# Kernel optimization log

Measured on AMD Instinct MI355X. Metric: run time of the kernel, lower is better.

The kernel has to match this reference:

```python
import jax, jax.numpy as jnp
import numpy as np

LN_EPS = 1e-5
BN_EPS = 1e-5
ATTN_EPS = 1e-6

def _ln(x, g, b):
    m = x.mean(-1, keepdims=True)
    v = x.var(-1, keepdims=True)
    return (x - m) / jnp.sqrt(v + LN_EPS) * g + b

def setup_inputs() -> dict:
    key = jax.random.key(0)
    ks = jax.random.split(key, 16)
    B, C, N = 4, 256, 8192
    s = 0.05
    def rn(k, shape, scale=1.0):
        return jax.random.normal(k, shape, jnp.float32) * scale
    return {
        "x1": rn(ks[0], (B, C, N)),
        "x2": rn(ks[1], (B, C, N)),
        "Wq": rn(ks[2], (C, C), s), "bq": rn(ks[3], (C,), s),
        "Wk": rn(ks[4], (C, C), s), "bk": rn(ks[5], (C,), s),
        "Wv": rn(ks[6], (C, C), s), "bv": rn(ks[7], (C,), s),
        "threshold": jnp.array([0.1], jnp.float32),
        "W1": rn(ks[8], (2 * C, 2 * C), s),
        "W2": rn(ks[9], (C, 2 * C), s),
        "g1": jnp.ones((C,), jnp.float32), "b1": jnp.zeros((C,), jnp.float32),
        "g2": jnp.ones((C,), jnp.float32), "b2": jnp.zeros((C,), jnp.float32),
        "Wa": rn(ks[10], (C, C), s), "ba": rn(ks[11], (C,), s),
        "bn_g": jnp.ones((C,), jnp.float32), "bn_b": jnp.zeros((C,), jnp.float32),
        "bn_m": jnp.zeros((C,), jnp.float32), "bn_v": jnp.ones((C,), jnp.float32),
    }

def reference(x1, x2, Wq, bq, Wk, bk, Wv, bv, threshold, W1, W2,
              g1, b1, g2, b2, Wa, ba, bn_g, bn_b, bn_m, bn_v):
    B, C, N = x1.shape
    H = 4
    d = C // H
    def conv1x1(x, W, b):  # nn.Conv1d(C, C, 1): [B,C,N] -> [B,C,N]
        return jnp.einsum('bcn,oc->bon', x, W) + b[:, None]
    # projections -> [B, N, H, d]
    q = conv1x1(x1, Wq, bq).transpose(0, 2, 1).reshape(B, N, H, d)
    k = conv1x1(x2, Wk, bk).transpose(0, 2, 1).reshape(B, N, H, d)
    v = conv1x1(x2, Wv, bv).transpose(0, 2, 1).reshape(B, N, H, d)
    # DynamicSparseLinearAttention
    Q = jax.nn.elu(q) + 1.0
    K = jax.nn.elu(k) + 1.0
    S = v.shape[1]
    vals = v / S
    KV = jnp.einsum('nshd,nshv->nhdv', K, vals)               # [B,H,d,d]
    scores = jnp.einsum('nlhd,nhd->nlh', Q, K.sum(axis=1))    # [B,N,H]
    sparse = jnp.where(scores > threshold[0], scores, 0.0)
    Z = 1.0 / (sparse + ATTN_EPS)
    msg = jnp.einsum('nlhd,nhdv,nlh->nlhv', Q, KV, Z) * S     # [B,N,H,d]
    # view [B,N,C]; the transpose(1,2).transpose(1,2) in torch cancels
    msg = msg.reshape(B, N, H * d)
    msg = _ln(msg, g1, b1)
    msg = jnp.concatenate([x1.transpose(0, 2, 1), msg], axis=2)  # [B,N,2C]
    msg = jax.nn.relu(msg @ W1.T) @ W2.T                         # [B,N,C]
    msg = _ln(msg, g2, b2).transpose(0, 2, 1)                    # [B,C,N]
    # aug shortcut: conv1x1 + BatchNorm1d (eval mode, running stats)
    aug = conv1x1(x1, Wa, ba)
    aug = (aug - bn_m[None, :, None]) / jnp.sqrt(bn_v[None, :, None] + BN_EPS)
    aug = aug * bn_g[None, :, None] + bn_b[None, :, None]
    return msg + x1 + aug
```

## Files before the change

### kernel.cpp

```cpp
#include <hip/hip_runtime.h>

#define BB 4
#define CC 256
#define NN 8192
#define HH 4
#define NCH 16

typedef unsigned short u16;
typedef __bf16 bf16x8 __attribute__((ext_vector_type(8)));
typedef float f32x4 __attribute__((ext_vector_type(4)));

__device__ __forceinline__ float bf2f(unsigned u) {
  return __uint_as_float(u << 16);
}
__device__ __forceinline__ u16 f2bf(float f) {
  unsigned u = __float_as_uint(f);
  return (u16)((u + 0x7fffu + ((u >> 16) & 1u)) >> 16);
}
__device__ __forceinline__ void bf8_to_f32(uint4 r, float* f) {
  f[0] = __uint_as_float(r.x << 16); f[1] = __uint_as_float(r.x & 0xffff0000u);
  f[2] = __uint_as_float(r.y << 16); f[3] = __uint_as_float(r.y & 0xffff0000u);
  f[4] = __uint_as_float(r.z << 16); f[5] = __uint_as_float(r.z & 0xffff0000u);
  f[6] = __uint_as_float(r.w << 16); f[7] = __uint_as_float(r.w & 0xffff0000u);
}
__device__ __forceinline__ void gload16(const u16* g, u16* l) {
  __builtin_amdgcn_global_load_lds(
      (const __attribute__((address_space(1))) unsigned int*)g,
      (__attribute__((address_space(3))) unsigned int*)l, 16, 0, 0);
}

__global__ __launch_bounds__(256) void cvt_all_kernel(
    const float* __restrict__ wq, const float* __restrict__ wk,
    const float* __restrict__ wv, const float* __restrict__ wa,
    const float* __restrict__ w1, const float* __restrict__ w2,
    u16* __restrict__ oq, u16* __restrict__ ok, u16* __restrict__ ov,
    u16* __restrict__ oa, u16* __restrict__ o1, u16* __restrict__ o2) {
  int i = blockIdx.x * 256 + threadIdx.x;
  const float* src;
  u16* dst;
  int off;
  if (i < 65536) { src = wq; dst = oq; off = i; }
  else if (i < 131072) { src = wk; dst = ok; off = i - 65536; }
  else if (i < 196608) { src = wv; dst = ov; off = i - 131072; }
  else if (i < 262144) { src = wa; dst = oa; off = i - 196608; }
  else if (i < 524288) { src = w1; dst = o1; off = i - 262144; }
  else { src = w2; dst = o2; off = i - 524288; }
  dst[off] = f2bf(src[off]);
}

__global__ __launch_bounds__(256) void transpose_kernel(const float* __restrict__ x1,
                                                        const float* __restrict__ x2,
                                                        u16* __restrict__ x1t,
                                                        u16* __restrict__ x2t) {
  __shared__ float T[64][65];
  const int bz = blockIdx.z;
  const int b = bz & 3;
  const float* x = (bz < 4) ? x1 : x2;
  u16* xt = (bz < 4) ? x1t : x2t;
  const int c0 = blockIdx.y * 64, n0 = blockIdx.x * 64;
  const float* xp = x + ((size_t)b * CC + c0) * NN + n0;
#pragma unroll
  for (int it = 0; it < 4; ++it) {
    int idx = threadIdx.x + it * 256;
    int r = idx >> 4, seg = idx & 15;
    float4 v = *(const float4*)(xp + (size_t)r * NN + seg * 4);
    T[r][seg * 4 + 0] = v.x; T[r][seg * 4 + 1] = v.y;
    T[r][seg * 4 + 2] = v.z; T[r][seg * 4 + 3] = v.w;
  }
  __syncthreads();
  u16* op = xt + ((size_t)b * NN + n0) * CC + c0;
  const int j = threadIdx.x >> 2, g = threadIdx.x & 3;
#pragma unroll
  for (int i = 0; i < 4; ++i) {
    int c = g * 16 + i * 4;
    uint2 pk;
    pk.x = (unsigned)f2bf(T[c + 0][j]) | ((unsigned)f2bf(T[c + 1][j]) << 16);
    pk.y = (unsigned)f2bf(T[c + 2][j]) | ((unsigned)f2bf(T[c + 3][j]) << 16);
    *(uint2*)(op + (size_t)j * CC + c) = pk;
  }
}

__global__ __launch_bounds__(256) void proj_all_kernel(
    const u16* __restrict__ x1t, const u16* __restrict__ x2t,
    const u16* __restrict__ Wqb, const u16* __restrict__ Wkb,
    const u16* __restrict__ Wvb, const u16* __restrict__ Wab,
    const float* __restrict__ bq, const float* __restrict__ bk,
    const float* __restrict__ bv, const float* __restrict__ ba,
    const float* __restrict__ bng, const float* __restrict__ bnb,
    const float* __restrict__ bnm, const float* __restrict__ bnv,
    u16* __restrict__ Qt, u16* __restrict__ K2, u16* __restrict__ V2,
    u16* __restrict__ augt) {
  __shared__ u16 As[128][72];
  __shared__ u16 Ws[128][72];
  const int mode = blockIdx.z;
  const u16* A = (mode == 0 || mode == 3) ? x1t : x2t;
  const u16* W = (mode == 0) ? Wqb : (mode == 1) ? Wkb : (mode == 2) ? Wvb : Wab;
  const float* bias = (mode == 0) ? bq : (mode == 1) ? bk : (mode == 2) ? bv : ba;
  u16* outp = (mode == 0) ? Qt : (mode == 1) ? K2 : (mode == 2) ? V2 : augt;
  const int m0 = blockIdx.x * 128, o0 = blockIdx.y * 128;
  const int tid = threadIdx.x, lane = tid & 63, wave = tid >> 6;
  const int wm = (wave >> 1) * 64, wo = (wave & 1) * 64;
  const int fr = lane & 15, fq = lane >> 4;
  f32x4 acc[4][4] = {};
  for (int kt = 0; kt < 4; ++kt) {
    const int k0 = kt << 6;
#pragma unroll
    for (int i = 0; i < 4; ++i) {
      int idx = tid + i * 256;
      int r = idx >> 3, s = idx & 7;
      *(uint4*)(&As[r][s * 8]) = *(const uint4*)(A + (size_t)(m0 + r) * CC + k0 + s * 8);
      *(uint4*)(&Ws[r][s * 8]) = *(const uint4*)(W + (size_t)(o0 + r) * CC + k0 + s * 8);
    }
    __syncthreads();
#pragma unroll
    for (int kk = 0; kk < 2; ++kk) {
      bf16x8 af[4], bfr[4];
#pragma unroll
      for (int mi = 0; mi < 4; ++mi)
        af[mi] = __builtin_bit_cast(bf16x8, *(const uint4*)(&As[wm + mi * 16 + fr][kk * 32 + fq * 8]));
#pragma unroll
      for (int oi = 0; oi < 4; ++oi)
        bfr[oi] = __builtin_bit_cast(bf16x8, *(const uint4*)(&Ws[wo + oi * 16 + fr][kk * 32 + fq * 8]));
#pragma unroll
      for (int mi = 0; mi < 4; ++mi)
#pragma unroll
        for (int oi = 0; oi < 4; ++oi)
          acc[mi][oi] = __builtin_amdgcn_mfma_f32_16x16x32_bf16(af[mi], bfr[oi], acc[mi][oi], 0, 0, 0);
    }
    __syncthreads();
  }
  const int bb_ = m0 >> 13;
  const int nb = m0 & (NN - 1);
#pragma unroll
  for (int oi = 0; oi < 4; ++oi) {
    const int col = o0 + wo + oi * 16 + fr;
    float b0 = bias[col], sc = 1.f, sh = 0.f;
    if (mode == 3) {
      sc = bng[col] * rsqrtf(bnv[col] + 1e-5f);
      sh = (b0 - bnm[col]) * sc + bnb[col];
    }
#pragma unroll
    for (int mi = 0; mi < 4; ++mi) {
      if (mode == 1 || mode == 2) {
        float v[4];
#pragma unroll
        for (int r = 0; r < 4; ++r) {
          float t = acc[mi][oi][r] + b0;
          if (mode == 1) t = (t > 0.f) ? (t + 1.f) : __expf(t);
          v[r] = t;
        }
        uint2 pk;
        pk.x = (unsigned)f2bf(v[0]) | ((unsigned)f2bf(v[1]) << 16);
        pk.y = (unsigned)f2bf(v[2]) | ((unsigned)f2bf(v[3]) << 16);
        const int nloc = nb + wm + mi * 16 + fq * 4;
        *(uint2*)(outp + ((size_t)bb_ * CC + col) * NN + nloc) = pk;
      } else {
        const int rowb = m0 + wm + mi * 16 + fq * 4;
#pragma unroll
        for (int r = 0; r < 4; ++r) {
          float v = acc[mi][oi][r];
          if (mode == 0) {
            v += b0;
            v = (v > 0.f) ? (v + 1.f) : __expf(v);
          } else {
            v = v * sc + sh;
          }
          outp[(size_t)(rowb + r) * CC + col] = f2bf(v);
        }
      }
    }
  }
}

__global__ __launch_bounds__(256) void kvpartial_kernel(const u16* __restrict__ K2,
                                                        const u16* __restrict__ V2,
                                                        float* __restrict__ Pkv,
                                                        float* __restrict__ Pks) {
  __shared__ u16 Ks[64 * 64];
  __shared__ u16 Vs[64 * 64];
  const int b = blockIdx.z, h = blockIdx.y, ch = blockIdx.x;
  const int tid = threadIdx.x, lane = tid & 63, w = tid >> 6;
  const int fr = lane & 15, fq = lane >> 4;
  const size_t base = ((size_t)b * CC + h * 64) * NN + (size_t)ch * (NN / NCH);
  f32x4 acc[4] = {};
  const int krow = tid >> 2, kq = tid & 3;
  float ksacc = 0.f;
  for (int step = 0; step < (NN / NCH) / 64; ++step) {
#pragma unroll
    for (int i = 0; i < 2; ++i) {
      int idx = tid + i * 256;
      int rr = idx >> 3, ss = idx & 7;
      gload16(K2 + base + (size_t)rr * NN + step * 64 + ss * 8, &Ks[(i * 256 + w * 64) * 8]);
      gload16(V2 + base + (size_t)rr * NN + step * 64 + ss * 8, &Vs[(i * 256 + w * 64) * 8]);
    }
    __syncthreads();
#pragma unroll
    for (int j = 0; j < 16; ++j) ksacc += bf2f(Ks[krow * 64 + kq * 16 + j]);
#pragma unroll
    for (int kk = 0; kk < 2; ++kk) {
      bf16x8 af = __builtin_bit_cast(bf16x8, *(const uint4*)(&Ks[(w * 16 + fr) * 64 + kk * 32 + fq * 8]));
#pragma unroll
      for (int oi = 0; oi < 4; ++oi) {
        bf16x8 bfr = __builtin_bit_cast(bf16x8, *(const uint4*)(&Vs[(oi * 16 + fr) * 64 + kk * 32 + fq * 8]));
        acc[oi] = __builtin_amdgcn_mfma_f32_16x16x32_bf16(af, bfr, acc[oi], 0, 0, 0);
      }
    }
    __syncthreads();
  }
  ksacc += __shfl_xor(ksacc, 1);
  ksacc += __shfl_xor(ksacc, 2);
  if (kq == 0) Pks[((size_t)ch * BB + b) * CC + h * 64 + krow] = ksacc;
  float* o = Pkv + (((size_t)ch * (BB * HH) + b * HH + h) << 12);
#pragma unroll
  for (int oi = 0; oi < 4; ++oi)
#pragma unroll
    for (int r = 0; r < 4; ++r)
      o[(w * 16 + fq * 4 + r) * 64 + oi * 16 + fr] = acc[oi][r];
}

__global__ __launch_bounds__(256) void kvreduce_kernel(const float* __restrict__ Pkv,
                                                       const float* __restrict__ Pks,
                                                       u16* __restrict__ KVT,
                                                       float* __restrict__ Ksum) {
  int i = blockIdx.x * 256 + threadIdx.x;
  int bh = i >> 12, dk = (i >> 6) & 63, dv = i & 63;
  float s = 0.f;
#pragma unroll
  for (int ch = 0; ch < NCH; ++ch)
    s += Pkv[(((size_t)ch * (BB * HH) + bh) << 12) + (dk << 6) + dv];
  KVT[((size_t)bh << 12) + (dv << 6) + dk] = f2bf(s);
  if (i < BB * CC) {
    float t = 0.f;
#pragma unroll
    for (int ch = 0; ch < NCH; ++ch) t += Pks[ch * (BB * CC) + i];
    Ksum[i] = t;
  }
}

__global__ __launch_bounds__(256) void bigmsg_kernel(const u16* __restrict__ Qt,
                                                     const u16* __restrict__ KVT,
                                                     const float* __restrict__ Ksum,
                                                     const float* __restrict__ thrp,
                                                     const float* __restrict__ g1,
                                                     const float* __restrict__ b1,
                                                     u16* __restrict__ msgN) {
  __shared__ u16 lds[64 * 264 + 4 * 64 * 72];
  __shared__ float Zs[64 * 4];
  u16* As = lds;
  u16* Ws = lds + 64 * 264;
  u16* Ml = lds;
  const int m0 = blockIdx.x * 64;
  const int b = blockIdx.z;
  const int tid = threadIdx.x, lane = tid & 63, w = tid >> 6;
  const int fr = lane & 15, fq = lane >> 4;
  const u16* Ap = Qt + ((size_t)b * NN + m0) * CC;
#pragma unroll
  for (int i = 0; i < 8; ++i) {
    int idx = tid + i * 256;
    int rr = idx >> 5, ss = idx & 31;
    *(uint4*)(&As[rr * 264 + ss * 8]) = *(const uint4*)(Ap + (size_t)rr * CC + ss * 8);
  }
  const u16* Wp = KVT + ((size_t)(b * HH) << 12);
#pragma unroll
  for (int i = 0; i < 8; ++i) {
    int idx = tid + i * 256;
    int h = idx >> 9, rr = (idx >> 3) & 63, ss = idx & 7;
    *(uint4*)(&Ws[(h * 64 + rr) * 72 + ss * 8]) = *(const uint4*)(Wp + ((size_t)h << 12) + rr * 64 + ss * 8);
  }
  __syncthreads();
  {
    const int row = tid >> 2, h = tid & 3;
    const float* ks = Ksum + b * CC + h * 64;
    float za = 0.f;
#pragma unroll
    for (int j8 = 0; j8 < 8; ++j8) {
      uint4 raw = *(const uint4*)(&As[row * 264 + h * 64 + j8 * 8]);
      float f[8];
      bf8_to_f32(raw, f);
#pragma unroll
      for (int j = 0; j < 8; ++j) za += f[j] * ks[j8 * 8 + j];
    }
    const float thrv = thrp[0];
    Zs[row * 4 + h] = 1.f / (((za > thrv) ? za : 0.f) + 1e-6f);
  }
  f32x4 acc[4][4] = {};
#pragma unroll
  for (int kk = 0; kk < 2; ++kk) {
    bf16x8 af[4], bfr[4];
#pragma unroll
    for (int mi = 0; mi < 4; ++mi)
      af[mi] = __builtin_bit_cast(bf16x8, *(const uint4*)(&As[(mi * 16 + fr) * 264 + w * 64 + kk * 32 + fq * 8]));
#pragma unroll
    for (int oi = 0; oi < 4; ++oi)
      bfr[oi] = __builtin_bit_cast(bf16x8, *(const uint4*)(&Ws[(w * 64 + oi * 16 + fr) * 72 + kk * 32 + fq * 8]));
#pragma unroll
    for (int mi = 0; mi < 4; ++mi)
#pragma unroll
      for (int oi = 0; oi < 4; ++oi)
        acc[mi][oi] = __builtin_amdgcn_mfma_f32_16x16x32_bf16(af[mi], bfr[oi], acc[mi][oi], 0, 0, 0);
  }
  __syncthreads();
#pragma unroll
  for (int oi = 0; oi < 4; ++oi) {
    const int col = w * 64 + oi * 16 + fr;
#pragma unroll
    for (int mi = 0; mi < 4; ++mi) {
#pragma unroll
      for (int r = 0; r < 4; ++r) {
        const int row = mi * 16 + fq * 4 + r;
        Ml[row * 272 + col] = f2bf(acc[mi][oi][r] * Zs[row * 4 + w]);
      }
    }
  }
  __syncthreads();
  {
    const int row = tid >> 2, q = tid & 3;
    const u16* mrow = &Ml[row * 272 + q * 64];
    float s1 = 0.f, s2 = 0.f;
#pragma unroll
    for (int j8 = 0; j8 < 8; ++j8) {
      uint4 raw = *(const uint4*)(mrow + j8 * 8);
      float f[8];
      bf8_to_f32(raw, f);
#pragma unroll
      for (int j = 0; j < 8; ++j) {
        s1 += f[j];
        s2 += f[j] * f[j];
      }
    }
    s1 += __shfl_xor(s1, 1); s2 += __shfl_xor(s2, 1);
    s1 += __shfl_xor(s1, 2); s2 += __shfl_xor(s2, 2);
    const float mean = s1 * (1.f / CC);
    const float var = s2 * (1.f / CC) - mean * mean;
    const float rs = rsqrtf(var + 1e-5f);
    u16* orow = msgN + ((size_t)b * NN + m0 + row) * CC + q * 64;
#pragma unroll
    for (int j8 = 0; j8 < 8; ++j8) {
      uint4 raw = *(const uint4*)(mrow + j8 * 8);
      float f[8];
      bf8_to_f32(raw, f);
      const int cb = q * 64 + j8 * 8;
      unsigned pk[4];
#pragma unroll
      for (int e = 0; e < 4; ++e) {
        float lo = (f[2 * e] - mean) * rs * g1[cb + 2 * e] + b1[cb + 2 * e];
        float hi = (f[2 * e + 1] - mean) * rs * g1[cb + 2 * e + 1] + b1[cb + 2 * e + 1];
        pk[e] = (unsigned)f2bf(lo) | ((unsigned)f2bf(hi) << 16);
      }
      *(uint4*)(orow + j8 * 8) = make_uint4(pk[0], pk[1], pk[2], pk[3]);
    }
  }
}

__global__ __launch_bounds__(256) void mlp1_kernel(const u16* __restrict__ A1,
                                                   const u16* __restrict__ A2,
                                                   const u16* __restrict__ W,
                                                   u16* __restrict__ outp) {
  __shared__ u16 As[128][72];
  __shared__ u16 Ws[128][72];
  const int m0 = blockIdx.x * 128, o0 = blockIdx.y * 128;
  const int tid = threadIdx.x, lane = tid & 63, wave = tid >> 6;
  const int wm = (wave >> 1) * 64, wo = (wave & 1) * 64;
  const int fr = lane & 15, fq = lane >> 4;
  f32x4 acc[4][4] = {};
  for (int kt = 0; kt < 8; ++kt) {
    const int k0 = kt << 6;
    const u16* Ap = (k0 < 256) ? (A1 + k0) : (A2 + (k0 - 256));
#pragma unroll
    for (int i = 0; i < 4; ++i) {
      int idx = tid + i * 256;
      int r = idx >> 3, s = idx & 7;
      *(uint4*)(&As[r][s * 8]) = *(const uint4*)(Ap + (size_t)(m0 + r) * CC + s * 8);
      *(uint4*)(&Ws[r][s * 8]) = *(const uint4*)(W + (size_t)(o0 + r) * 512 + k0 + s * 8);
    }
    __syncthreads();
#pragma unroll
    for (int kk = 0; kk < 2; ++kk) {
      bf16x8 af[4], bfr[4];
#pragma unroll
      for (int mi = 0; mi < 4; ++mi)
        af[mi] = __builtin_bit_cast(bf16x8, *(const uint4*)(&As[wm + mi * 16 + fr][kk * 32 + fq * 8]));
#pragma unroll
      for (int oi = 0; oi < 4; ++oi)
        bfr[oi] = __builtin_bit_cast(bf16x8, *(const uint4*)(&Ws[wo + oi * 16 + fr][kk * 32 + fq * 8]));
#pragma unroll
      for (int mi = 0; mi < 4; ++mi)
#pragma unroll
        for (int oi = 0; oi < 4; ++oi)
          acc[mi][oi] = __builtin_amdgcn_mfma_f32_16x16x32_bf16(af[mi], bfr[oi], acc[mi][oi], 0, 0, 0);
    }
    __syncthreads();
  }
#pragma unroll
  for (int oi = 0; oi < 4; ++oi) {
    const int col = o0 + wo + oi * 16 + fr;
#pragma unroll
    for (int mi = 0; mi < 4; ++mi) {
      const int rowb = m0 + wm + mi * 16 + fq * 4;
#pragma unroll
      for (int r = 0; r < 4; ++r)
        outp[(size_t)(rowb + r) * 512 + col] = f2bf(fmaxf(acc[mi][oi][r], 0.f));
    }
  }
}

__global__ __launch_bounds__(512) void mlp2fused_kernel(const u16* __restrict__ h1,
                                                        const u16* __restrict__ W2b,
                                                        const u16* __restrict__ augt,
                                                        const float* __restrict__ x1,
                                                        const float* __restrict__ g2,
                                                        const float* __restrict__ b2,
                                                        float* __restrict__ outp) {
  __shared__ u16 lds[128 * 272];
  u16* As = lds;
  u16* Ws = lds + 128 * 72;
  u16* Tl = lds;
  const int m0 = blockIdx.x * 128;
  const int b = m0 >> 13, nb = m0 & (NN - 1);
  const int tid = threadIdx.x, lane = tid & 63, w = tid >> 6;
  const int wm = (w >> 2) * 64, wo = (w & 3) * 64;
  const int fr = lane & 15, fq = lane >> 4;
  f32x4 acc[4][4] = {};
  for (int kt = 0; kt < 8; ++kt) {
    const int k0 = kt << 6;
#pragma unroll
    for (int i = 0; i < 2; ++i) {
      int idx = tid + i * 512;
      int rr = idx >> 3, ss = idx & 7;
      *(uint4*)(&As[rr * 72 + ss * 8]) = *(const uint4*)(h1 + (size_t)(m0 + rr) * 512 + k0 + ss * 8);
    }
#pragma unroll
    for (int i = 0; i < 4; ++i) {
      int idx = tid + i * 512;
      int rr = idx >> 3, ss = idx & 7;
      *(uint4*)(&Ws[rr * 72 + ss * 8]) = *(const uint4*)(W2b + (size_t)rr * 512 + k0 + ss * 8);
    }
    __syncthreads();
#pragma unroll
    for (int kk = 0; kk < 2; ++kk) {
      bf16x8 af[4], bfr[4];
#pragma unroll
      for (int mi = 0; mi < 4; ++mi)
        af[mi] = __builtin_bit_cast(bf16x8, *(const uint4*)(&As[(wm + mi * 16 + fr) * 72 + kk * 32 + fq * 8]));
#pragma unroll
      for (int oi = 0; oi < 4; ++oi)
        bfr[oi] = __builtin_bit_cast(bf16x8, *(const uint4*)(&Ws[(wo + oi * 16 + fr) * 72 + kk * 32 + fq * 8]));
#pragma unroll
      for (int mi = 0; mi < 4; ++mi)
#pragma unroll
        for (int oi = 0; oi < 4; ++oi)
          acc[mi][oi] = __builtin_amdgcn_mfma_f32_16x16x32_bf16(af[mi], bfr[oi], acc[mi][oi], 0, 0, 0);
    }
    __syncthreads();
  }
#pragma unroll
  for (int oi = 0; oi < 4; ++oi) {
    const int col = wo + oi * 16 + fr;
#pragma unroll
    for (int mi = 0; mi < 4; ++mi) {
#pragma unroll
      for (int r = 0; r < 4; ++r) {
        const int row = wm + mi * 16 + fq * 4 + r;
        Tl[row * 272 + col] = f2bf(acc[mi][oi][r]);
      }
    }
  }
  __syncthreads();
  {
    const int row = tid >> 2, q = tid & 3;
    u16* mrow = &Tl[row * 272 + q * 64];
    float s1 = 0.f, s2 = 0.f;
#pragma unroll
    for (int j8 = 0; j8 < 8; ++j8) {
      uint4 raw = *(const uint4*)(mrow + j8 * 8);
      float f[8];
      bf8_to_f32(raw, f);
#pragma unroll
      for (int j = 0; j < 8; ++j) {
        s1 += f[j];
        s2 += f[j] * f[j];
      }
    }
    s1 += __shfl_xor(s1, 1); s2 += __shfl_xor(s2, 1);
    s1 += __shfl_xor(s1, 2); s2 += __shfl_xor(s2, 2);
    const float mean = s1 * (1.f / CC);
    const float var = s2 * (1.f / CC) - mean * mean;
    const float rs = rsqrtf(var + 1e-5f);
    const u16* arow = augt + ((size_t)b * NN + nb + row) * CC + q * 64;
#pragma unroll
    for (int j8 = 0; j8 < 8; ++j8) {
      uint4 raw = *(const uint4*)(mrow + j8 * 8);
      uint4 ar = *(const uint4*)(arow + j8 * 8);
      float f[8], af[8];
      bf8_to_f32(raw, f);
      bf8_to_f32(ar, af);
      const int cb = q * 64 + j8 * 8;
      unsigned pk[4];
#pragma unroll
      for (int e = 0; e < 4; ++e) {
        float lo = (f[2 * e] - mean) * rs * g2[cb + 2 * e] + b2[cb + 2 * e] + af[2 * e];
        float hi = (f[2 * e + 1] - mean) * rs * g2[cb + 2 * e + 1] + b2[cb + 2 * e + 1] + af[2 * e + 1];
        pk[e] = (unsigned)f2bf(lo) | ((unsigned)f2bf(hi) << 16);
      }
      *(uint4*)(mrow + j8 * 8) = make_uint4(pk[0], pk[1], pk[2], pk[3]);
    }
  }
  __syncthreads();
#pragma unroll
  for (int i = 0; i < 64; ++i) {
    int idx = tid + i * 512;
    int n = idx & 127, c = idx >> 7;
    size_t off = ((size_t)b * CC + c) * NN + nb + n;
    outp[off] = bf2f(Tl[n * 272 + c]) + x1[off];
  }
}

extern "C" void kernel_launch(void* const* d_in, const int* in_sizes, int n_in,
                              void* d_out, int out_size, void* d_ws, size_t ws_size,
                              hipStream_t stream) {
  (void)in_sizes; (void)n_in; (void)out_size; (void)ws_size;
  const float* x1 = (const float*)d_in[0];
  const float* x2 = (const float*)d_in[1];
  const float* Wq = (const float*)d_in[2];
  const float* bq = (const float*)d_in[3];
  const float* Wk = (const float*)d_in[4];
  const float* bk = (const float*)d_in[5];
  const float* Wv = (const float*)d_in[6];
  const float* bv = (const float*)d_in[7];
  const float* thr = (const float*)d_in[8];
  const float* W1 = (const float*)d_in[9];
  const float* W2 = (const float*)d_in[10];
  const float* g1 = (const float*)d_in[11];
  const float* b1 = (const float*)d_in[12];
  const float* g2 = (const float*)d_in[13];
  const float* b2 = (const float*)d_in[14];
  const float* Wa = (const float*)d_in[15];
  const float* ba = (const float*)d_in[16];
  const float* bng = (const float*)d_in[17];
  const float* bnb = (const float*)d_in[18];
  const float* bnm = (const float*)d_in[19];
  const float* bnv = (const float*)d_in[20];
  float* out = (float*)d_out;

  char* ws = (char*)d_ws;
  constexpr size_t SZ = (size_t)BB * NN * CC * sizeof(u16);
  u16* x1t = (u16*)(ws);
  u16* x2t = (u16*)(ws + SZ);
  u16* Qt = (u16*)(ws + 2 * SZ);
  u16* K2 = (u16*)(ws + 3 * SZ);
  u16* V2 = (u16*)(ws + 4 * SZ);
  u16* augt = (u16*)(ws + 5 * SZ);
  float* Pkv = (float*)(ws + 6 * SZ);
  u16* h1 = Qt;
  u16* msgN = V2;
  char* tail = ws + 7 * SZ;
  float* Ksum = (float*)tail;
  u16* KVT = (u16*)(tail + 4096);
  float* Pks = (float*)(tail + 4096 + 131072);
  u16* Wqb = (u16*)(tail + 4096 + 131072 + 65536);
  u16* Wkb = Wqb + CC * CC;
  u16* Wvb = Wkb + CC * CC;
  u16* Wab = Wvb + CC * CC;
  u16* W1b = Wab + CC * CC;
  u16* W2b = W1b + 512 * 512;

  cvt_all_kernel<<<dim3(2560), 256, 0, stream>>>(Wq, Wk, Wv, Wa, W1, W2,
                                                 Wqb, Wkb, Wvb, Wab, W1b, W2b);
  transpose_kernel<<<dim3(NN / 64, CC / 64, 2 * BB), 256, 0, stream>>>(x1, x2, x1t, x2t);
  proj_all_kernel<<<dim3(256, 2, 4), 256, 0, stream>>>(
      x1t, x2t, Wqb, Wkb, Wvb, Wab, bq, bk, bv, ba, bng, bnb, bnm, bnv,
      Qt, K2, V2, augt);
  kvpartial_kernel<<<dim3(NCH, HH, BB), 256, 0, stream>>>(K2, V2, Pkv, Pks);
  kvreduce_kernel<<<dim3(256), 256, 0, stream>>>(Pkv, Pks, KVT, Ksum);
  bigmsg_kernel<<<dim3(NN / 64, 1, BB), 256, 0, stream>>>(Qt, KVT, Ksum, thr, g1, b1, msgN);
  mlp1_kernel<<<dim3(256, 4), 256, 0, stream>>>(x1t, msgN, W1b, h1);
  mlp2fused_kernel<<<dim3(256), 512, 0, stream>>>(h1, W2b, augt, x1, g2, b2, out);
}
```

Measured before the change: 184.9 us.

## Read GEMM weight fragments from global and stage epilogue stores through LDS

In the projection, MLP1 and MLP2 GEMM kernels, the weight tile is no longer staged in shared memory. Each wave reads its B fragments straight from global memory, relying on the small weight matrices staying cached. The projection and MLP1 epilogues now write results into a padded LDS tile and then issue coalesced 16-byte global stores, replacing scattered 2-byte or 8-byte stores. The trade is less LDS traffic and footprint, which may raise occupancy, against global-memory latency on the MFMA operand loads inside the inner loop.

```diff
diff --git a/kernel.cpp b/kernel.cpp
--- a/kernel.cpp
+++ b/kernel.cpp
@@ -90,8 +90,9 @@
     const float* __restrict__ bnm, const float* __restrict__ bnv,
     u16* __restrict__ Qt, u16* __restrict__ K2, u16* __restrict__ V2,
     u16* __restrict__ augt) {
-  __shared__ u16 As[128][72];
-  __shared__ u16 Ws[128][72];
+  __shared__ u16 lds[128 * 132];
+  u16* As = lds;
+  u16* T = lds;
   const int mode = blockIdx.z;
   const u16* A = (mode == 0 || mode == 3) ? x1t : x2t;
   const u16* W = (mode == 0) ? Wqb : (mode == 1) ? Wkb : (mode == 2) ? Wvb : Wab;
@@ -108,8 +109,7 @@
     for (int i = 0; i < 4; ++i) {
       int idx = tid + i * 256;
       int r = idx >> 3, s = idx & 7;
-      *(uint4*)(&As[r][s * 8]) = *(const uint4*)(A + (size_t)(m0 + r) * CC + k0 + s * 8);
-      *(uint4*)(&Ws[r][s * 8]) = *(const uint4*)(W + (size_t)(o0 + r) * CC + k0 + s * 8);
+      *(uint4*)(&As[r * 72 + s * 8]) = *(const uint4*)(A + (size_t)(m0 + r) * CC + k0 + s * 8);
     }
     __syncthreads();
 #pragma unroll
@@ -117,10 +117,10 @@
       bf16x8 af[4], bfr[4];
 #pragma unroll
       for (int mi = 0; mi < 4; ++mi)
-        af[mi] = __builtin_bit_cast(bf16x8, *(const uint4*)(&As[wm + mi * 16 + fr][kk * 32 + fq * 8]));
+        af[mi] = __builtin_bit_cast(bf16x8, *(const uint4*)(&As[(wm + mi * 16 + fr) * 72 + kk * 32 + fq * 8]));
 #pragma unroll
       for (int oi = 0; oi < 4; ++oi)
-        bfr[oi] = __builtin_bit_cast(bf16x8, *(const uint4*)(&Ws[wo + oi * 16 + fr][kk * 32 + fq * 8]));
+        bfr[oi] = __builtin_bit_cast(bf16x8, *(const uint4*)(W + (size_t)(o0 + wo + oi * 16 + fr) * CC + k0 + kk * 32 + fq * 8));
 #pragma unroll
       for (int mi = 0; mi < 4; ++mi)
 #pragma unroll
@@ -133,7 +133,8 @@
   const int nb = m0 & (NN - 1);
 #pragma unroll
   for (int oi = 0; oi < 4; ++oi) {
-    const int col = o0 + wo + oi * 16 + fr;
+    const int o_loc = wo + oi * 16 + fr;
+    const int col = o0 + o_loc;
     float b0 = bias[col], sc = 1.f, sh = 0.f;
     if (mode == 3) {
       sc = bng[col] * rsqrtf(bnv[col] + 1e-5f);
@@ -141,33 +142,43 @@
     }
 #pragma unroll
     for (int mi = 0; mi < 4; ++mi) {
+      const int mbase = wm + mi * 16 + fq * 4;
+      float v[4];
+#pragma unroll
+      for (int r = 0; r < 4; ++r) {
+        float t = acc[mi][oi][r];
+        if (mode == 0 || mode == 1) {
+          t += b0;
+          t = (t > 0.f) ? (t + 1.f) : __expf(t);
+        } else if (mode == 2) {
+          t += b0;
+        } else {
+          t = t * sc + sh;
+        }
+        v[r] = t;
+      }
       if (mode == 1 || mode == 2) {
-        float v[4];
-#pragma unroll
-        for (int r = 0; r < 4; ++r) {
-          float t = acc[mi][oi][r] + b0;
-          if (mode == 1) t = (t > 0.f) ? (t + 1.f) : __expf(t);
-          v[r] = t;
+#pragma unroll
+        for (int e = 0; e < 2; ++e) {
+          unsigned pk = (unsigned)f2bf(v[2 * e]) | ((unsigned)f2bf(v[2 * e + 1]) << 16);
+          *(unsigned*)(&T[o_loc * 132 + mbase + 2 * e]) = pk;
         }
-        uint2 pk;
-        pk.x = (unsigned)f2bf(v[0]) | ((unsigned)f2bf(v[1]) << 16);
-        pk.y = (unsigned)f2bf(v[2]) | ((unsigned)f2bf(v[3]) << 16);
-        const int nloc = nb + wm + mi * 16 + fq * 4;
-        *(uint2*)(outp + ((size_t)bb_ * CC + col) * NN + nloc) = pk;
       } else {
-        const int rowb = m0 + wm + mi * 16 + fq * 4;
-#pragma unroll
-        for (int r = 0; r < 4; ++r) {
-          float v = acc[mi][oi][r];
-          if (mode == 0) {
-            v += b0;
-            v = (v > 0.f) ? (v + 1.f) : __expf(v);
-          } else {
-            v = v * sc + sh;
-          }
-          outp[(size_t)(rowb + r) * CC + col] = f2bf(v);
-        }
-      }
+#pragma unroll
+        for (int r = 0; r < 4; ++r) T[(mbase + r) * 132 + o_loc] = f2bf(v[r]);
+      }
+    }
+  }
+  __syncthreads();
+#pragma unroll
+  for (int i = 0; i < 8; ++i) {
+    int idx = tid + i * 256;
+    int r = idx >> 4, c = (idx & 15) * 8;
+    uint4 d = *(const uint4*)(&T[r * 132 + c]);
+    if (mode == 1 || mode == 2) {
+      *(uint4*)(outp + ((size_t)bb_ * CC + o0 + r) * NN + nb + c) = d;
+    } else {
+      *(uint4*)(outp + (size_t)(m0 + r) * CC + o0 + c) = d;
     }
   }
 }
@@ -356,8 +367,9 @@
                                                    const u16* __restrict__ A2,
                                                    const u16* __restrict__ W,
                                                    u16* __restrict__ outp) {
-  __shared__ u16 As[128][72];
-  __shared__ u16 Ws[128][72];
+  __shared__ u16 lds[128 * 132];
+  u16* As = lds;
+  u16* T = lds;
   const int m0 = blockIdx.x * 128, o0 = blockIdx.y * 128;
   const int tid = threadIdx.x, lane = tid & 63, wave = tid >> 6;
   const int wm = (wave >> 1) * 64, wo = (wave & 1) * 64;
@@ -370,8 +382,7 @@
     for (int i = 0; i < 4; ++i) {
       int idx = tid + i * 256;
       int r = idx >> 3, s = idx & 7;
-      *(uint4*)(&As[r][s * 8]) = *(const uint4*)(Ap + (size_t)(m0 + r) * CC + s * 8);
-      *(uint4*)(&Ws[r][s * 8]) = *(const uint4*)(W + (size_t)(o0 + r) * 512 + k0 + s * 8);
+      *(uint4*)(&As[r * 72 + s * 8]) = *(const uint4*)(Ap + (size_t)(m0 + r) * CC + s * 8);
     }
     __syncthreads();
 #pragma unroll
@@ -379,10 +390,10 @@
       bf16x8 af[4], bfr[4];
 #pragma unroll
       for (int mi = 0; mi < 4; ++mi)
-        af[mi] = __builtin_bit_cast(bf16x8, *(const uint4*)(&As[wm + mi * 16 + fr][kk * 32 + fq * 8]));
+        af[mi] = __builtin_bit_cast(bf16x8, *(const uint4*)(&As[(wm + mi * 16 + fr) * 72 + kk * 32 + fq * 8]));
 #pragma unroll
       for (int oi = 0; oi < 4; ++oi)
-        bfr[oi] = __builtin_bit_cast(bf16x8, *(const uint4*)(&Ws[wo + oi * 16 + fr][kk * 32 + fq * 8]));
+        bfr[oi] = __builtin_bit_cast(bf16x8, *(const uint4*)(W + (size_t)(o0 + wo + oi * 16 + fr) * 512 + k0 + kk * 32 + fq * 8));
 #pragma unroll
       for (int mi = 0; mi < 4; ++mi)
 #pragma unroll
@@ -393,14 +404,21 @@
   }
 #pragma unroll
   for (int oi = 0; oi < 4; ++oi) {
-    const int col = o0 + wo + oi * 16 + fr;
+    const int o_loc = wo + oi * 16 + fr;
 #pragma unroll
     for (int mi = 0; mi < 4; ++mi) {
-      const int rowb = m0 + wm + mi * 16 + fq * 4;
+      const int mbase = wm + mi * 16 + fq * 4;
 #pragma unroll
       for (int r = 0; r < 4; ++r)
-        outp[(size_t)(rowb + r) * 512 + col] = f2bf(fmaxf(acc[mi][oi][r], 0.f));
-    }
+        T[(mbase + r) * 132 + o_loc] = f2bf(fmaxf(acc[mi][oi][r], 0.f));
+    }
+  }
+  __syncthreads();
+#pragma unroll
+  for (int i = 0; i < 8; ++i) {
+    int idx = tid + i * 256;
+    int r = idx >> 4, c = (idx & 15) * 8;
+    *(uint4*)(outp + (size_t)(m0 + r) * 512 + o0 + c) = *(const uint4*)(&T[r * 132 + c]);
   }
 }
 
@@ -413,7 +431,6 @@
                                                         float* __restrict__ outp) {
   __shared__ u16 lds[128 * 272];
   u16* As = lds;
-  u16* Ws = lds + 128 * 72;
   u16* Tl = lds;
   const int m0 = blockIdx.x * 128;
   const int b = m0 >> 13, nb = m0 & (NN - 1);
@@ -429,12 +446,6 @@
       int rr = idx >> 3, ss = idx & 7;
       *(uint4*)(&As[rr * 72 + ss * 8]) = *(const uint4*)(h1 + (size_t)(m0 + rr) * 512 + k0 + ss * 8);
     }
-#pragma unroll
-    for (int i = 0; i < 4; ++i) {
-      int idx = tid + i * 512;
-      int rr = idx >> 3, ss = idx & 7;
-      *(uint4*)(&Ws[rr * 72 + ss * 8]) = *(const uint4*)(W2b + (size_t)rr * 512 + k0 + ss * 8);
-    }
     __syncthreads();
 #pragma unroll
     for (int kk = 0; kk < 2; ++kk) {
@@ -444,7 +455,7 @@
         af[mi] = __builtin_bit_cast(bf16x8, *(const uint4*)(&As[(wm + mi * 16 + fr) * 72 + kk * 32 + fq * 8]));
 #pragma unroll
       for (int oi = 0; oi < 4; ++oi)
-        bfr[oi] = __builtin_bit_cast(bf16x8, *(const uint4*)(&Ws[(wo + oi * 16 + fr) * 72 + kk * 32 + fq * 8]));
+        bfr[oi] = __builtin_bit_cast(bf16x8, *(const uint4*)(W2b + (size_t)(wo + oi * 16 + fr) * 512 + k0 + kk * 32 + fq * 8));
 #pragma unroll
       for (int mi = 0; mi < 4; ++mi)
 #pragma unroll
```

Result: slower. 218.2 us (+18.0%).
